# Optimization experiments

Measured on AMD Instinct MI355X. Metric: run time of the kernel, lower is better.

## Reference

```python
import jax, jax.numpy as jnp
from jax import lax
import numpy as np

K = 3  # kernel size per dim
P = 1  # padding per dim
DN = ('NCDHW', 'OIDHW', 'NCDHW')  # conv3d dimension numbers


def setup_inputs() -> dict:
    key = jax.random.key(0)
    k1, k2 = jax.random.split(key)
    x = jax.random.normal(k1, (2, 16, 24, 24, 24, 24), dtype=jnp.float32)
    # Full 4D kernel [out_c, in_c, k0, k1, k2, k3]; the torch module stores it as
    # k0 separate Conv3d layers with weights W[:, :, i] each.
    W = jax.random.normal(k2, (32, 16, K, K, K, K), dtype=jnp.float32) * 0.05
    return {"x": x, "W": W}


def _conv4d(x, W):
    # x: [b, c_in, D0, D1, D2, D3]; W: [c_out, c_in, K, K, K, K]
    # 'same' 4D conv (stride 1, pad 1, k 3), decomposed over the leading
    # kernel dim into K conv3d calls (same math as the torch module, where
    # frame_results[j - i] += Conv3d_i(x_padded[:, :, j]) ).
    b, c, D0, D1, D2, D3 = x.shape
    c_out = W.shape[0]
    xp = jnp.pad(x, ((0, 0), (0, 0), (P, P), (P, P), (P, P), (P, P)))
    O0 = D0  # stride 1, pad 1, k 3 -> same size
    out = None
    for i in range(K):
        xs = xp[:, :, i:i + O0]                               # [b,c,O0,D1+2,D2+2,D3+2]
        xs = xs.transpose(0, 2, 1, 3, 4, 5).reshape(
            b * O0, c, D1 + 2 * P, D2 + 2 * P, D3 + 2 * P)    # fold frame dim into batch
        o = lax.conv_general_dilated(xs, W[:, :, i], (1, 1, 1), 'VALID',
                                     dimension_numbers=DN)    # [b*O0, c_out, D1, D2, D3]
        o = o.reshape(b, O0, c_out, D1, D2, D3).transpose(0, 2, 1, 3, 4, 5)
        out = o if out is None else out + o
    return out


def reference(x, W):
    return _conv4d(x, W)
```

## Files before the change

### kernel.cpp

```cpp
#include <hip/hip_runtime.h>


#define D      24
#define D2_    (24*24)
#define D3_    (24*24*24)
#define D4_    (24*24*24*24)
#define CIN    16
#define COUT   32
#define DP     26
#define TPW    3
#define NTHR   384
#define GRID   256
#define NTILES (2*24*24)

#define XT_ELEMS  (2*24*26*26*26*16)
#define XT_BYTES  (XT_ELEMS*2)
#define WT_ELEMS  (81*32*16)
#define CNT_OFF_B (XT_BYTES + WT_ELEMS*2)
#define WS_NEED   (CNT_OFF_B + 64)

typedef __bf16 bf16x8 __attribute__((ext_vector_type(8)));
typedef float  f32x16 __attribute__((ext_vector_type(16)));
typedef unsigned short ushort_t;
typedef ushort_t ushort8 __attribute__((ext_vector_type(8)));
typedef ushort_t ushort4_ __attribute__((ext_vector_type(4)));

union u2b8 { ushort8 u; bf16x8 b; };

typedef const __attribute__((address_space(1))) unsigned int gu32;
typedef __attribute__((address_space(3))) unsigned int lu32;

__device__ inline ushort_t f2bf(float f) {
    union { float f; unsigned u; } x; x.f = f;
    unsigned r = x.u + 0x7FFFu + ((x.u >> 16) & 1u);
    return (ushort_t)(r >> 16);
}

__global__ __launch_bounds__(NTHR) void conv4d_fused(
    const float* __restrict__ x,
    const float* __restrict__ W,
    float* __restrict__ out,
    ushort_t* __restrict__ ws)
{
    __shared__ __align__(16) ushort_t slab[2][DP * DP * CIN];

    ushort_t* xt = ws;
    ushort_t* Wt = ws + XT_BYTES / 2;
    unsigned* cnt = (unsigned*)((char*)ws + CNT_OFF_B);

    const int bk  = blockIdx.x;
    const int tid = threadIdx.x;

    {
        const long gtid = (long)bk * NTHR + tid;
        const long nthr = (long)GRID * NTHR;
        for (long u = gtid; u < XT_ELEMS / 8; u += nthr) {
            const int  h   = (int)(u & 1);
            long pos = u >> 1;
            const int p3 = (int)(pos % 26); pos /= 26;
            const int p2 = (int)(pos % 26); pos /= 26;
            const int p1 = (int)(pos % 26); pos /= 26;
            const int d0 = (int)(pos % 24);
            const int b  = (int)(pos / 24);
            const int r1 = p1 - 1, r2 = p2 - 1, r3 = p3 - 1;
            ushort8 v;
            if ((unsigned)r1 < 24u && (unsigned)r2 < 24u && (unsigned)r3 < 24u) {
                const float* xp = x + (long)(b * 16 + h * 8) * D4_
                                    + d0 * D3_ + r1 * D2_ + r2 * D + r3;
                #pragma unroll
                for (int c = 0; c < 8; ++c) v[c] = f2bf(xp[(long)c * D4_]);
            } else {
                #pragma unroll
                for (int c = 0; c < 8; ++c) v[c] = 0;
            }
            *(ushort8*)&xt[u * 8] = v;
        }
        for (long i = gtid; i < WT_ELEMS; i += nthr) {
            const int tap = (int)(i >> 9);
            const int co  = (int)((i >> 4) & 31);
            const int ci  = (int)(i & 15);
            Wt[i] = f2bf(W[((long)co * 16 + ci) * 81 + tap]);
        }
    }

    __threadfence();
    __syncthreads();
    if (tid == 0) {
        __hip_atomic_fetch_add(cnt, 1u, __ATOMIC_ACQ_REL, __HIP_MEMORY_SCOPE_AGENT);
        while (__hip_atomic_load(cnt, __ATOMIC_ACQUIRE, __HIP_MEMORY_SCOPE_AGENT)
               < (unsigned)GRID)
            __builtin_amdgcn_s_sleep(2);
    }
    __syncthreads();

    const int lane = tid & 63;
    const int wave = tid >> 6;
    const int col  = lane & 31;
    const int hi   = lane >> 5;

    int ppos[TPW], sbase[TPW];
    #pragma unroll
    for (int t = 0; t < TPW; ++t) {
        const int pos = (wave * TPW + t) * 32 + col;
        const int d2  = pos / D;
        const int d3  = pos - d2 * D;
        ppos[t]  = pos;
        sbase[t] = (d2 * DP + d3) * CIN + hi * 8;
    }

    int buf = 0;
    for (int tile = bk; tile < NTILES; tile += GRID) {
        const int b   = tile / 576;
        const int d01 = tile % 576;
        const int d0  = d01 / 24;
        const int d1  = d01 % 24;

        f32x16 acc[TPW];
        #pragma unroll
        for (int t = 0; t < TPW; ++t)
            #pragma unroll
            for (int r = 0; r < 16; ++r) acc[t][r] = 0.f;

        const int k0lo = (d0 == 0) ? 1 : 0;
        const int k0hi = (d0 == 23) ? 1 : 2;
        const int nb   = (k0hi - k0lo + 1) * 3;

        auto stage = [&](int sb, int i) {
            const int k0 = k0lo + i / 3;
            const int k1 = i % 3;
            const int r0 = d0 + k0 - 1;
            const ushort_t* src = xt + (((long)b * 24 + r0) * 26 + (d1 + k1))
                                       * (676 * 16);
            ushort_t* dst = &slab[sb][0];
            for (int c = wave; c < 22; c += 6) {
                const bool act = (c < 21) | (lane < 8);
                if (act)
                    __builtin_amdgcn_global_load_lds(
                        (gu32*)(src) + (c * 256 + lane * 4),
                        (lu32*)(dst + c * 512), 16, 0, 0);
            }
        };

        __syncthreads();
        stage(buf, 0);

        for (int i = 0; i < nb; ++i) {
            __syncthreads();
            if (i + 1 < nb) stage(buf ^ 1, i + 1);

            const int k0 = k0lo + i / 3;
            const int k1 = i % 3;
            const int tapg = (k0 * 3 + k1) * 9;

            bf16x8 af[9];
            #pragma unroll
            for (int kc = 0; kc < 9; ++kc) {
                u2b8 cvt;
                cvt.u = *(const ushort8*)&Wt[((long)(tapg + kc) * 32 + col) * 16
                                             + hi * 8];
                af[kc] = cvt.b;
            }

            #pragma unroll
            for (int kc = 0; kc < 9; ++kc) {
                const int k2 = kc / 3, k3 = kc - 3 * (kc / 3);
                const int koff = (k2 * DP + k3) * CIN;
                #pragma unroll
                for (int t = 0; t < TPW; ++t) {
                    u2b8 cvt;
                    cvt.u = *(const ushort8*)&slab[buf][sbase[t] + koff];
                    acc[t] = __builtin_amdgcn_mfma_f32_32x32x16_bf16(
                                 af[kc], cvt.b, acc[t], 0, 0, 0);
                }
            }
            buf ^= 1;
        }

        float* ob = out + (long)b * COUT * D4_ + (long)d0 * D3_ + (long)d1 * D2_;
        #pragma unroll
        for (int t = 0; t < TPW; ++t) {
            #pragma unroll
            for (int r = 0; r < 16; ++r) {
                const int co = (r & 3) + 8 * (r >> 2) + 4 * hi;
                ob[(long)co * D4_ + ppos[t]] = acc[t][r];
            }
        }
    }
}

__device__ inline int fswz(int f) { return f ^ ((f >> 3) & 7); }

__global__ __launch_bounds__(NTHR) void conv4d_mfma_fb(
    const float* __restrict__ x,
    const float* __restrict__ W,
    float* __restrict__ out)
{
    __shared__ __align__(16) ushort_t slab[DP * DP * CIN];
    __shared__ __align__(16) ushort_t agrp[9 * COUT * CIN];

    const int d01  = blockIdx.x;
    const int b    = blockIdx.y;
    const int d0   = d01 / D;
    const int d1   = d01 % D;
    const int tid  = threadIdx.x;
    const int lane = tid & 63;
    const int wave = tid >> 6;
    const int col  = lane & 31;
    const int hi   = lane >> 5;

    const int afbase = fswz(col * 2 + hi) * 8;
    int ppos[TPW], sbase[TPW];
    #pragma unroll
    for (int t = 0; t < TPW; ++t) {
        int pos = (wave * TPW + t) * 32 + col;
        int d2  = pos / D;
        int d3  = pos - d2 * D;
        ppos[t]  = pos;
        sbase[t] = (d2 * DP + d3) * CIN + hi * 8;
    }

    f32x16 acc[TPW];
    #pragma unroll
    for (int t = 0; t < TPW; ++t)
        #pragma unroll
        for (int r = 0; r < 16; ++r) acc[t][r] = 0.f;

    const float* xb = x + (long)b * CIN * D4_;

    for (int k0 = 0; k0 < 3; ++k0) {
        const int r0 = d0 + k0 - 1;
        if ((unsigned)r0 >= (unsigned)D) continue;
        for (int k1 = 0; k1 < 3; ++k1) {
            const int r1 = d1 + k1 - 1;
            if ((unsigned)r1 >= (unsigned)D) continue;

            __syncthreads();

            const float* xp = xb + (long)r0 * D3_ + (long)r1 * D2_;
            for (int idx = tid; idx < DP * DP * 2; idx += NTHR) {
                const int pidx = idx >> 1;
                const int h    = idx & 1;
                const int p2   = pidx / DP;
                const int p3   = pidx - p2 * DP;
                const int s2   = p2 - 1;
                const int s3   = p3 - 1;
                const bool in  = (unsigned)s2 < (unsigned)D &&
                                 (unsigned)s3 < (unsigned)D;
                const float* xs = xp + s2 * D + s3;
                ushort8 v;
                #pragma unroll
                for (int c = 0; c < 8; ++c) {
                    float f = in ? xs[(long)(h * 8 + c) * D4_] : 0.f;
                    v[c] = f2bf(f);
                }
                *(ushort8*)&slab[idx * 8] = v;
            }

            const int kw0 = k0 * 27 + k1 * 9;
            for (int u = tid; u < 9 * COUT * 4; u += NTHR) {
                const int tap = u >> 7;
                const int rem = u & 127;
                const int co  = rem >> 2;
                const int q   = rem & 3;
                const int ci0 = (q >> 1) * 8 + (q & 1) * 4;
                const float* wp = W + co * (CIN * 81) + kw0 + tap;
                ushort4_ v;
                #pragma unroll
                for (int c = 0; c < 4; ++c)
                    v[c] = f2bf(wp[(ci0 + c) * 81]);
                const int f  = co * 2 + (q >> 1);
                const int h2 = q & 1;
                *(ushort4_*)&agrp[tap * 512 + fswz(f) * 8 + h2 * 4] = v;
            }
            __syncthreads();

            bf16x8 af[9];
            #pragma unroll
            for (int kc = 0; kc < 9; ++kc) {
                u2b8 cvt;
                cvt.u = *(const ushort8*)&agrp[kc * 512 + afbase];
                af[kc] = cvt.b;
            }

            #pragma unroll
            for (int kc = 0; kc < 9; ++kc) {
                const int k2 = kc / 3, k3 = kc - 3 * (kc / 3);
                const int koff = (k2 * DP + k3) * CIN;
                #pragma unroll
                for (int t = 0; t < TPW; ++t) {
                    u2b8 cvt;
                    cvt.u = *(const ushort8*)&slab[sbase[t] + koff];
                    acc[t] = __builtin_amdgcn_mfma_f32_32x32x16_bf16(
                                 af[kc], cvt.b, acc[t], 0, 0, 0);
                }
            }
        }
    }

    float* ob = out + (long)b * COUT * D4_ + (long)d0 * D3_ + (long)d1 * D2_;
    #pragma unroll
    for (int t = 0; t < TPW; ++t) {
        #pragma unroll
        for (int r = 0; r < 16; ++r) {
            const int co = (r & 3) + 8 * (r >> 2) + 4 * hi;
            ob[(long)co * D4_ + ppos[t]] = acc[t][r];
        }
    }
}

extern "C" void kernel_launch(void* const* d_in, const int* in_sizes, int n_in,
                              void* d_out, int out_size, void* d_ws, size_t ws_size,
                              hipStream_t stream)
{
    const float* x = (const float*)d_in[0];
    const float* W = (const float*)d_in[1];
    float* out     = (float*)d_out;

    if (ws_size >= (size_t)WS_NEED) {
        hipMemsetAsync((char*)d_ws + CNT_OFF_B, 0, 64, stream);
        hipLaunchKernelGGL(conv4d_fused, dim3(GRID), dim3(NTHR), 0, stream,
                           x, W, out, (ushort_t*)d_ws);
    } else {
        hipLaunchKernelGGL(conv4d_mfma_fb, dim3(D * D, 2), dim3(NTHR), 0, stream,
                           x, W, out);
    }
}
```

Baseline: 177.9 us.

## Triple-buffer LDS slabs with fine-grained vmcnt waits and 9-wave blocks

Moves the fused conv kernel from double to triple-buffered LDS staging, with a prefetch distance of two. The __syncthreads calls are replaced by explicit s_waitcnt vmcnt counts plus s_barrier. Weight fragments are double-buffered in registers, and MFMA sections are wrapped in s_setprio. Blocks grow to 9 waves of 2 tiles each (576 threads), which gives more waves per tile for latency hiding. The aim is to overlap global-to-LDS loads with MFMA work. The hand-tuned vmcnt counts are fragile and depend on how many loads each wave issues, so a wrong count could silently race.

```diff
diff --git a/kernel.cpp b/kernel.cpp
--- a/kernel.cpp
+++ b/kernel.cpp
@@ -8,10 +8,11 @@
 #define CIN    16
 #define COUT   32
 #define DP     26
-#define TPW    3
-#define NTHR   384
+#define TPW    2
+#define NTHR   576
 #define GRID   256
 #define NTILES (2*24*24)
+#define SLABU  (DP*DP*CIN)
 
 #define XT_ELEMS  (2*24*26*26*26*16)
 #define XT_BYTES  (XT_ELEMS*2)
@@ -42,7 +43,7 @@
     float* __restrict__ out,
     ushort_t* __restrict__ ws)
 {
-    __shared__ __align__(16) ushort_t slab[2][DP * DP * CIN];
+    __shared__ __align__(16) ushort_t slab[3][SLABU];
 
     ushort_t* xt = ws;
     ushort_t* Wt = ws + XT_BYTES / 2;
@@ -55,7 +56,7 @@
         const long gtid = (long)bk * NTHR + tid;
         const long nthr = (long)GRID * NTHR;
         for (long u = gtid; u < XT_ELEMS / 8; u += nthr) {
-            const int  h   = (int)(u & 1);
+            const int h = (int)(u & 1);
             long pos = u >> 1;
             const int p3 = (int)(pos % 26); pos /= 26;
             const int p2 = (int)(pos % 26); pos /= 26;
@@ -97,6 +98,7 @@
     const int wave = tid >> 6;
     const int col  = lane & 31;
     const int hi   = lane >> 5;
+    ushort_t* slabflat = &slab[0][0];
 
     int ppos[TPW], sbase[TPW];
     #pragma unroll
@@ -108,7 +110,6 @@
         sbase[t] = (d2 * DP + d3) * CIN + hi * 8;
     }
 
-    int buf = 0;
     for (int tile = bk; tile < NTILES; tile += GRID) {
         const int b   = tile / 576;
         const int d01 = tile % 576;
@@ -125,56 +126,84 @@
         const int k0hi = (d0 == 23) ? 1 : 2;
         const int nb   = (k0hi - k0lo + 1) * 3;
 
-        auto stage = [&](int sb, int i) {
-            const int k0 = k0lo + i / 3;
-            const int k1 = i % 3;
+        auto stage = [&](int sb2, int body) {
+            const int k0 = k0lo + body / 3, k1 = body % 3;
             const int r0 = d0 + k0 - 1;
             const ushort_t* src = xt + (((long)b * 24 + r0) * 26 + (d1 + k1))
-                                       * (676 * 16);
-            ushort_t* dst = &slab[sb][0];
-            for (int c = wave; c < 22; c += 6) {
-                const bool act = (c < 21) | (lane < 8);
-                if (act)
-                    __builtin_amdgcn_global_load_lds(
-                        (gu32*)(src) + (c * 256 + lane * 4),
-                        (lu32*)(dst + c * 512), 16, 0, 0);
+                                       * (long)SLABU;
+            ushort_t* dst = slabflat + sb2 * SLABU;
+            #pragma unroll
+            for (int j = 0; j < 3; ++j) {
+                const int c = wave + 9 * j;
+                if (c < 22) {
+                    const bool act = (c < 21) | (lane < 8);
+                    if (act)
+                        __builtin_amdgcn_global_load_lds(
+                            (gu32*)src + (c * 256 + lane * 4),
+                            (lu32*)(dst + c * 512), 16, 0, 0);
+                }
             }
         };
 
-        __syncthreads();
-        stage(buf, 0);
-
-        for (int i = 0; i < nb; ++i) {
-            __syncthreads();
-            if (i + 1 < nb) stage(buf ^ 1, i + 1);
-
-            const int k0 = k0lo + i / 3;
-            const int k1 = i % 3;
-            const int tapg = (k0 * 3 + k1) * 9;
-
-            bf16x8 af[9];
+        auto loadaf = [&](bf16x8* af, int body) {
+            const int k0 = k0lo + body / 3, k1 = body % 3;
+            const ushort_t* w = Wt + ((k0 * 3 + k1) * 9) * 512 + col * 16 + hi * 8;
             #pragma unroll
             for (int kc = 0; kc < 9; ++kc) {
-                u2b8 cvt;
-                cvt.u = *(const ushort8*)&Wt[((long)(tapg + kc) * 32 + col) * 16
-                                             + hi * 8];
+                u2b8 cvt; cvt.u = *(const ushort8*)(w + kc * 512);
                 af[kc] = cvt.b;
             }
-
+        };
+
+        auto compute = [&](const bf16x8* af, const ushort_t* sbuf) {
+            __builtin_amdgcn_s_setprio(1);
             #pragma unroll
             for (int kc = 0; kc < 9; ++kc) {
-                const int k2 = kc / 3, k3 = kc - 3 * (kc / 3);
-                const int koff = (k2 * DP + k3) * CIN;
+                const int koff = ((kc / 3) * DP + (kc % 3)) * CIN;
                 #pragma unroll
                 for (int t = 0; t < TPW; ++t) {
                     u2b8 cvt;
-                    cvt.u = *(const ushort8*)&slab[buf][sbase[t] + koff];
+                    cvt.u = *(const ushort8*)&sbuf[sbase[t] + koff];
                     acc[t] = __builtin_amdgcn_mfma_f32_32x32x16_bf16(
                                  af[kc], cvt.b, acc[t], 0, 0, 0);
                 }
             }
-            buf ^= 1;
-        }
+            __builtin_amdgcn_s_setprio(0);
+        };
+
+        bf16x8 afA[9], afB[9];
+
+        stage(0, 0);
+        stage(1, 1);
+        loadaf(afA, 0);
+
+        int sb = 0;
+        for (int i = 0; i < nb; ++i) {
+            if (i == 0) {
+                if (wave < 4) asm volatile("s_waitcnt vmcnt(12)" ::: "memory");
+                else          asm volatile("s_waitcnt vmcnt(11)" ::: "memory");
+            } else if (i < nb - 1) {
+                if (wave < 4) asm volatile("s_waitcnt vmcnt(21)" ::: "memory");
+                else          asm volatile("s_waitcnt vmcnt(20)" ::: "memory");
+            } else {
+                asm volatile("s_waitcnt vmcnt(18)" ::: "memory");
+            }
+            asm volatile("s_barrier" ::: "memory");
+
+            const int sb2 = (sb == 0) ? 2 : sb - 1;
+            if (i + 2 < nb) stage(sb2, i + 2);
+
+            const ushort_t* sbuf = slabflat + sb * SLABU;
+            if (i & 1) {
+                if (i + 1 < nb) loadaf(afA, i + 1);
+                compute(afB, sbuf);
+            } else {
+                if (i + 1 < nb) loadaf(afB, i + 1);
+                compute(afA, sbuf);
+            }
+            sb = (sb == 2) ? 0 : sb + 1;
+        }
+        asm volatile("s_barrier" ::: "memory");
 
         float* ob = out + (long)b * COUT * D4_ + (long)d0 * D3_ + (long)d1 * D2_;
         #pragma unroll
@@ -190,7 +219,7 @@
 
 __device__ inline int fswz(int f) { return f ^ ((f >> 3) & 7); }
 
-__global__ __launch_bounds__(NTHR) void conv4d_mfma_fb(
+__global__ __launch_bounds__(384) void conv4d_mfma_fb(
     const float* __restrict__ x,
     const float* __restrict__ W,
     float* __restrict__ out)
@@ -209,19 +238,19 @@
     const int hi   = lane >> 5;
 
     const int afbase = fswz(col * 2 + hi) * 8;
-    int ppos[TPW], sbase[TPW];
+    int ppos[3], sbase[3];
     #pragma unroll
-    for (int t = 0; t < TPW; ++t) {
-        int pos = (wave * TPW + t) * 32 + col;
+    for (int t = 0; t < 3; ++t) {
+        int pos = (wave * 3 + t) * 32 + col;
         int d2  = pos / D;
         int d3  = pos - d2 * D;
         ppos[t]  = pos;
         sbase[t] = (d2 * DP + d3) * CIN + hi * 8;
     }
 
-    f32x16 acc[TPW];
+    f32x16 acc[3];
     #pragma unroll
-    for (int t = 0; t < TPW; ++t)
+    for (int t = 0; t < 3; ++t)
         #pragma unroll
         for (int r = 0; r < 16; ++r) acc[t][r] = 0.f;
 
@@ -237,7 +266,7 @@
             __syncthreads();
 
             const float* xp = xb + (long)r0 * D3_ + (long)r1 * D2_;
-            for (int idx = tid; idx < DP * DP * 2; idx += NTHR) {
+            for (int idx = tid; idx < DP * DP * 2; idx += 384) {
                 const int pidx = idx >> 1;
                 const int h    = idx & 1;
                 const int p2   = pidx / DP;
@@ -257,7 +286,7 @@
             }
 
             const int kw0 = k0 * 27 + k1 * 9;
-            for (int u = tid; u < 9 * COUT * 4; u += NTHR) {
+            for (int u = tid; u < 9 * COUT * 4; u += 384) {
                 const int tap = u >> 7;
                 const int rem = u & 127;
                 const int co  = rem >> 2;
@@ -287,7 +316,7 @@
                 const int k2 = kc / 3, k3 = kc - 3 * (kc / 3);
                 const int koff = (k2 * DP + k3) * CIN;
                 #pragma unroll
-                for (int t = 0; t < TPW; ++t) {
+                for (int t = 0; t < 3; ++t) {
                     u2b8 cvt;
                     cvt.u = *(const ushort8*)&slab[sbase[t] + koff];
                     acc[t] = __builtin_amdgcn_mfma_f32_32x32x16_bf16(
@@ -299,7 +328,7 @@
 
     float* ob = out + (long)b * COUT * D4_ + (long)d0 * D3_ + (long)d1 * D2_;
     #pragma unroll
-    for (int t = 0; t < TPW; ++t) {
+    for (int t = 0; t < 3; ++t) {
         #pragma unroll
         for (int r = 0; r < 16; ++r) {
             const int co = (r & 3) + 8 * (r >> 2) + 4 * hi;
@@ -321,7 +350,7 @@
         hipLaunchKernelGGL(conv4d_fused, dim3(GRID), dim3(NTHR), 0, stream,
                            x, W, out, (ushort_t*)d_ws);
     } else {
-        hipLaunchKernelGGL(conv4d_mfma_fb, dim3(D * D, 2), dim3(NTHR), 0, stream,
+        hipLaunchKernelGGL(conv4d_mfma_fb, dim3(D * D, 2), dim3(384), 0, stream,
                            x, W, out);
     }
 }
```

Measured after the change: 287.4 us. +61.5%, slower.
